# Kernel optimization log

Hardware: AMD Instinct MI355X
Metric: run time of the kernel (lower is better)

The kernel has to match this reference:

```python
import jax, jax.numpy as jnp
import numpy as np

HEADS = 4
OUT_DIM = 32
NUM_NODES = 10000
NUM_EDGES = 640000  # avg degree 64


def setup_inputs() -> dict:
    key = jax.random.key(0)
    k1, k2, k3, k4 = jax.random.split(key, 4)
    HE = HEADS * NUM_EDGES
    x_i = jax.random.normal(k1, (HE, OUT_DIM), dtype=jnp.float32)
    x_j = jax.random.normal(k2, (HE, OUT_DIM), dtype=jnp.float32)
    # glorot init for a: [heads, 1, 2*out_dim]
    fan = 1 + 2 * OUT_DIM
    limit = np.sqrt(6.0 / fan)
    a = jax.random.uniform(k3, (HEADS, 1, 2 * OUT_DIM), dtype=jnp.float32,
                           minval=-limit, maxval=limit)
    # edge_index[1] holds per-head-offset destination node ids in [0, heads*num_nodes)
    edge_index = jax.random.randint(k4, (2, HE), 0, HEADS * NUM_NODES, dtype=jnp.int64)
    return {"x_i": x_i, "x_j": x_j, "a": a, "edge_index": edge_index,
            "num_nodes": NUM_NODES}


def reference(x_i, x_j, a, edge_index, num_nodes):
    heads = a.shape[0]
    two_d = a.shape[2]
    E = x_i.shape[0] // heads
    # cat features, reshape to [heads, E, 2D]
    e_ = jnp.concatenate([x_i, x_j], axis=1).reshape(heads, E, two_d)
    # per-head score: mm(e_[h], a[h].T) -> [E, 1]; vectorized over heads
    scores = jnp.einsum("hed,hd->he", e_, a[:, 0, :])  # [heads, E]
    e = jax.nn.leaky_relu(scores, 0.2).reshape(heads * E, 1)
    # segment softmax over destination ids (PyG-style)
    idx = edge_index[1]
    num_seg = num_nodes * heads
    seg_max = jax.ops.segment_max(e, idx, num_segments=num_seg)  # [num_seg, 1]
    out = jnp.exp(e - seg_max[idx])
    seg_sum = jax.ops.segment_sum(out, idx, num_segments=num_seg)
    return out / (seg_sum[idx] + 1e-16)
```

## Files before the change

### kernel.cpp

```cpp
#include <hip/hip_runtime.h>


#define LRELU_SLOPE 0.2f

__global__ void score_exp_kernel(const float* __restrict__ x_i,
                                 const float* __restrict__ x_j,
                                 const float* __restrict__ a,
                                 const int* __restrict__ idx,
                                 float* __restrict__ p_out,
                                 float* __restrict__ seg_sum,
                                 int HE, int E, int a_len) {
    __shared__ float a_sh[512];
    int t = threadIdx.x;
    if (t < a_len) a_sh[t] = a[t];
    __syncthreads();

    int lane = t & 63;
    int wave = t >> 6;
    int sub  = lane & 7;
    int rl   = lane >> 3;
    int r = blockIdx.x * 32 + wave * 8 + rl;
    if (r >= HE) return;

    int h = r / E;
    const float4 xi = *(const float4*)(x_i + (size_t)r * 32 + sub * 4);
    const float4 xj = *(const float4*)(x_j + (size_t)r * 32 + sub * 4);
    const float4 a1 = *(const float4*)(a_sh + h * 64 + sub * 4);
    const float4 a2 = *(const float4*)(a_sh + h * 64 + 32 + sub * 4);

    float p = xi.x * a1.x + xi.y * a1.y + xi.z * a1.z + xi.w * a1.w
            + xj.x * a2.x + xj.y * a2.y + xj.z * a2.z + xj.w * a2.w;
    p += __shfl_xor(p, 1);
    p += __shfl_xor(p, 2);
    p += __shfl_xor(p, 4);

    if (sub == 0) {
        float s = (p > 0.0f) ? p : LRELU_SLOPE * p;
        float pe = expf(s);
        p_out[r] = pe;
        atomicAdd(&seg_sum[idx[r]], pe);
    }
}

__global__ void norm_kernel(const int* __restrict__ idx,
                            const float* __restrict__ seg_sum,
                            float* __restrict__ inout, int HE) {
    int r = blockIdx.x * blockDim.x + threadIdx.x;
    if (r >= HE) return;
    inout[r] = inout[r] / (seg_sum[idx[r]] + 1e-16f);
}

extern "C" void kernel_launch(void* const* d_in, const int* in_sizes, int n_in,
                              void* d_out, int out_size, void* d_ws, size_t ws_size,
                              hipStream_t stream) {
    const float* x_i = (const float*)d_in[0];
    const float* x_j = (const float*)d_in[1];
    const float* a   = (const float*)d_in[2];
    const int* edge_index = (const int*)d_in[3];
    const int num_nodes = 10000;

    const int HE    = in_sizes[0] / 32;
    const int a_len = in_sizes[2];
    const int heads = a_len / 64;
    const int E     = HE / heads;
    const int num_seg = heads * num_nodes;

    const int* idx = edge_index + HE;
    float* out = (float*)d_out;
    float* seg_sum = (float*)d_ws;

    hipMemsetAsync(seg_sum, 0, (size_t)num_seg * sizeof(float), stream);
    hipLaunchKernelGGL(score_exp_kernel, dim3((HE + 31) / 32), dim3(256),
                       0, stream, x_i, x_j, a, idx, out, seg_sum, HE, E, a_len);
    hipLaunchKernelGGL(norm_kernel, dim3((HE + 255) / 256), dim3(256),
                       0, stream, idx, seg_sum, out, HE);
}
```

Measured before the change: 647.5 us.

## Privatize segment sums in LDS per block and reduce partials instead of global atomics

Replaces per-edge global atomicAdd into the segment-sum array with a persistent 256-block kernel. Each block holds a full 40000-entry segment histogram in LDS, accumulates with LDS atomics, then writes its partial to workspace. A separate kernel reduces the partials into seg_sum, and normalization is vectorized to float4/int4. The aim is to remove contended global atomics, at the cost of extra partial-buffer traffic, a large LDS footprint limiting occupancy to one block per CU, and a fallback path for other shapes.

```diff
diff --git a/kernel.cpp b/kernel.cpp
--- a/kernel.cpp
+++ b/kernel.cpp
@@ -2,14 +2,89 @@
 
 
 #define LRELU_SLOPE 0.2f
+#define NSEG 40000
+#define NPART 256
+#define TPB_A 1024
+#define ROWS_PER_BLK 128
 
-__global__ void score_exp_kernel(const float* __restrict__ x_i,
-                                 const float* __restrict__ x_j,
-                                 const float* __restrict__ a,
-                                 const int* __restrict__ idx,
-                                 float* __restrict__ p_out,
-                                 float* __restrict__ seg_sum,
-                                 int HE, int E, int a_len) {
+__global__ __launch_bounds__(TPB_A, 1)
+void score_part_kernel(const float* __restrict__ x_i,
+                       const float* __restrict__ x_j,
+                       const float* __restrict__ a,
+                       const int* __restrict__ idx,
+                       float* __restrict__ p_out,
+                       float* __restrict__ partials,
+                       int HE, int E, int a_len, int nchunks) {
+    extern __shared__ float seg_lds[];
+    __shared__ float a_sh[512];
+    int t = threadIdx.x;
+    if (t < a_len) a_sh[t] = a[t];
+    for (int i = t; i < NSEG; i += TPB_A) seg_lds[i] = 0.0f;
+    __syncthreads();
+
+    int sub = t & 7;
+    int rl  = t >> 3;
+
+    for (int c = blockIdx.x; c < nchunks; c += NPART) {
+        int r = c * ROWS_PER_BLK + rl;
+        if (r < HE) {
+            int h = r / E;
+            const float4 xi = *(const float4*)(x_i + (size_t)r * 32 + sub * 4);
+            const float4 xj = *(const float4*)(x_j + (size_t)r * 32 + sub * 4);
+            const float4 a1 = *(const float4*)(a_sh + h * 64 + sub * 4);
+            const float4 a2 = *(const float4*)(a_sh + h * 64 + 32 + sub * 4);
+
+            float p = xi.x * a1.x + xi.y * a1.y + xi.z * a1.z + xi.w * a1.w
+                    + xj.x * a2.x + xj.y * a2.y + xj.z * a2.z + xj.w * a2.w;
+            p += __shfl_xor(p, 1);
+            p += __shfl_xor(p, 2);
+            p += __shfl_xor(p, 4);
+
+            if (sub == 0) {
+                float s = (p > 0.0f) ? p : LRELU_SLOPE * p;
+                float pe = expf(s);
+                p_out[r] = pe;
+                atomicAdd(&seg_lds[idx[r]], pe);
+            }
+        }
+    }
+    __syncthreads();
+    float* dst = partials + (size_t)blockIdx.x * NSEG;
+    for (int i = t; i < NSEG; i += TPB_A) dst[i] = seg_lds[i];
+}
+
+__global__ void reduce_kernel(const float* __restrict__ partials,
+                              float* __restrict__ seg_sum) {
+    int tseg = blockIdx.x * blockDim.x + threadIdx.x;
+    if (tseg >= NSEG) return;
+    const float* p = partials + tseg;
+    float s = 0.0f;
+#pragma unroll 8
+    for (int b = 0; b < NPART; ++b) s += p[(size_t)b * NSEG];
+    seg_sum[tseg] = s;
+}
+
+__global__ void norm4_kernel(const int4* __restrict__ idx4,
+                             const float* __restrict__ seg_sum,
+                             float4* __restrict__ inout4, int n4) {
+    int i = blockIdx.x * blockDim.x + threadIdx.x;
+    if (i >= n4) return;
+    float4 p = inout4[i];
+    int4 id = idx4[i];
+    p.x = p.x / (seg_sum[id.x] + 1e-16f);
+    p.y = p.y / (seg_sum[id.y] + 1e-16f);
+    p.z = p.z / (seg_sum[id.z] + 1e-16f);
+    p.w = p.w / (seg_sum[id.w] + 1e-16f);
+    inout4[i] = p;
+}
+
+__global__ void score_exp_atomic_kernel(const float* __restrict__ x_i,
+                                        const float* __restrict__ x_j,
+                                        const float* __restrict__ a,
+                                        const int* __restrict__ idx,
+                                        float* __restrict__ p_out,
+                                        float* __restrict__ seg_sum,
+                                        int HE, int E, int a_len) {
     __shared__ float a_sh[512];
     int t = threadIdx.x;
     if (t < a_len) a_sh[t] = a[t];
@@ -42,14 +117,6 @@
     }
 }
 
-__global__ void norm_kernel(const int* __restrict__ idx,
-                            const float* __restrict__ seg_sum,
-                            float* __restrict__ inout, int HE) {
-    int r = blockIdx.x * blockDim.x + threadIdx.x;
-    if (r >= HE) return;
-    inout[r] = inout[r] / (seg_sum[idx[r]] + 1e-16f);
-}
-
 extern "C" void kernel_launch(void* const* d_in, const int* in_sizes, int n_in,
                               void* d_out, int out_size, void* d_ws, size_t ws_size,
                               hipStream_t stream) {
@@ -67,11 +134,32 @@
 
     const int* idx = edge_index + HE;
     float* out = (float*)d_out;
-    float* seg_sum = (float*)d_ws;
 
-    hipMemsetAsync(seg_sum, 0, (size_t)num_seg * sizeof(float), stream);
-    hipLaunchKernelGGL(score_exp_kernel, dim3((HE + 31) / 32), dim3(256),
-                       0, stream, x_i, x_j, a, idx, out, seg_sum, HE, E, a_len);
-    hipLaunchKernelGGL(norm_kernel, dim3((HE + 255) / 256), dim3(256),
-                       0, stream, idx, seg_sum, out, HE);
+    float* seg_sum  = (float*)d_ws;
+    float* partials = (float*)d_ws + 40960;
+    size_t need = (40960 + (size_t)NPART * NSEG) * sizeof(float);
+
+    const int nchunks = (HE + ROWS_PER_BLK - 1) / ROWS_PER_BLK;
+
+    if (num_seg == NSEG && ws_size >= need) {
+        static bool attr_set = false;
+        if (!attr_set) {
+            (void)hipFuncSetAttribute((const void*)score_part_kernel,
+                                      hipFuncAttributeMaxDynamicSharedMemorySize,
+                                      NSEG * (int)sizeof(float));
+            attr_set = true;
+        }
+        hipLaunchKernelGGL(score_part_kernel, dim3(NPART), dim3(TPB_A),
+                           NSEG * sizeof(float), stream,
+                           x_i, x_j, a, idx, out, partials, HE, E, a_len, nchunks);
+        hipLaunchKernelGGL(reduce_kernel, dim3((NSEG + 255) / 256), dim3(256),
+                           0, stream, partials, seg_sum);
+    } else {
+        hipMemsetAsync(seg_sum, 0, (size_t)num_seg * sizeof(float), stream);
+        hipLaunchKernelGGL(score_exp_atomic_kernel, dim3((HE + 31) / 32), dim3(256),
+                           0, stream, x_i, x_j, a, idx, out, seg_sum, HE, E, a_len);
+    }
+
+    hipLaunchKernelGGL(norm4_kernel, dim3((HE / 4 + 255) / 256), dim3(256),
+                       0, stream, (const int4*)idx, seg_sum, (float4*)out, HE / 4);
 }
```

Result: slower. 674.3 us (+4.1%).
